# Kernel tuning notes

Hardware: AMD Instinct MI355X
Metric: run time of the kernel (lower is better)

Reference implementation:

```python
import jax, jax.numpy as jnp
import numpy as np
import math

B, T, E, H = 64, 256, 1024, 16
HD = E // H  # 64
EPS = 1e-5


def layernorm(x, g, b):
    mu = jnp.mean(x, axis=-1, keepdims=True)
    var = jnp.mean(jnp.square(x - mu), axis=-1, keepdims=True)
    return (x - mu) * jax.lax.rsqrt(var + EPS) * g + b


def setup_inputs() -> dict:
    key = jax.random.key(0)
    ks = jax.random.split(key, 10)
    s = 0.02
    return {
        "x": jax.random.normal(ks[0], (B, T, E), dtype=jnp.float32),
        "ln1_g": jnp.ones((E,), jnp.float32),
        "ln1_b": jnp.zeros((E,), jnp.float32),
        "wk": jax.random.normal(ks[1], (H, E, HD), jnp.float32) * s,
        "wq": jax.random.normal(ks[2], (H, E, HD), jnp.float32) * s,
        "wv": jax.random.normal(ks[3], (H, E, HD), jnp.float32) * s,
        "w_proj": jax.random.normal(ks[4], (E, E), jnp.float32) * s,
        "b_proj": jnp.zeros((E,), jnp.float32),
        "ln2_g": jnp.ones((E,), jnp.float32),
        "ln2_b": jnp.zeros((E,), jnp.float32),
        "w1": jax.random.normal(ks[5], (E, E), jnp.float32) * s,
        "b1": jnp.zeros((E,), jnp.float32),
        "w2": jax.random.normal(ks[6], (E, E), jnp.float32) * s,
        "b2": jnp.zeros((E,), jnp.float32),
    }


def reference(x, ln1_g, ln1_b, wk, wq, wv, w_proj, b_proj, ln2_g, ln2_b, w1, b1, w2, b2):
    # --- multi-head causal attention on LN1(x) ---
    h = layernorm(x, ln1_g, ln1_b)
    k = jnp.einsum('bte,hed->bhtd', h, wk)
    q = jnp.einsum('bte,hed->bhtd', h, wq)
    v = jnp.einsum('bte,hed->bhtd', h, wv)
    # NOTE: original computes k @ q^T (K.Q^T), not the standard Q.K^T -- kept faithful
    scores = jnp.einsum('bhtd,bhsd->bhts', k, q) / math.sqrt(HD)
    mask = jnp.tril(jnp.ones((T, T), dtype=bool))
    scores = jnp.where(mask, scores, -jnp.inf)
    attn_w = jax.nn.softmax(scores, axis=-1)  # dropout = identity in eval
    attn = jnp.einsum('bhts,bhsd->bhtd', attn_w, v)
    attn = attn.transpose(0, 2, 1, 3).reshape(B, T, E)  # concat heads
    x = x + attn @ w_proj + b_proj
    # --- feed-forward on LN2(x) ---
    h2 = layernorm(x, ln2_g, ln2_b)
    ff = jax.nn.relu(h2 @ w1 + b1) @ w2 + b2
    return x + ff
```

## Files before the change

### kernel.cpp

```cpp
#include <hip/hip_runtime.h>

typedef unsigned int u32;
typedef unsigned short u16;
typedef __attribute__((ext_vector_type(8))) short bf16x8;
typedef __attribute__((ext_vector_type(4))) float f32x4;

#define GLOBAL_AS __attribute__((address_space(1)))
#define LDS_AS    __attribute__((address_space(3)))

#define B_   64
#define T_   256
#define E_   1024
#define H_   16
#define HD_  64
#define NTOK (B_*T_)
#define K_   1024
#define LNEPS 1e-5f

__device__ __forceinline__ float bflo(u32 u){ return __uint_as_float(u << 16); }
__device__ __forceinline__ float bfhi(u32 u){ return __uint_as_float(u & 0xffff0000u); }
__device__ __forceinline__ u16 f2bf(float f){
  u32 x = __float_as_uint(f);
  u32 r = x + 0x7fffu + ((x >> 16) & 1u);
  return (u16)(r >> 16);
}
__device__ __forceinline__ u16 f2bf_trunc(float f){
  return (u16)(__float_as_uint(f) >> 16);
}
__device__ __forceinline__ u32 pack2(float a, float b){
  return (u32)f2bf(a) | ((u32)f2bf(b) << 16);
}

__device__ __forceinline__ void gload16(const u16* g, u16* l){
  __builtin_amdgcn_global_load_lds((const GLOBAL_AS void*)g, (LDS_AS void*)l, 16, 0, 0);
}

__global__ __launch_bounds__(256) void ln_bf16_kernel(
    const float* __restrict__ x, const float* __restrict__ g,
    const float* __restrict__ b, u16* __restrict__ o)
{
  int lane  = threadIdx.x & 63;
  int token = (blockIdx.x << 2) + (threadIdx.x >> 6);
  const float4* xr = (const float4*)(x + (size_t)token * E_);
  float4 v[4];
  float s = 0.f, ss = 0.f;
  #pragma unroll
  for (int i = 0; i < 4; ++i){
    v[i] = xr[lane + 64 * i];
    s += v[i].x + v[i].y + v[i].z + v[i].w;
    ss = fmaf(v[i].x, v[i].x, fmaf(v[i].y, v[i].y,
         fmaf(v[i].z, v[i].z, fmaf(v[i].w, v[i].w, ss))));
  }
  #pragma unroll
  for (int off = 32; off > 0; off >>= 1){
    s  += __shfl_xor(s,  off);
    ss += __shfl_xor(ss, off);
  }
  float mu   = s * (1.f / E_);
  float var  = ss * (1.f / E_) - mu * mu;
  float rstd = rsqrtf(var + LNEPS);
  const float4* gr = (const float4*)g;
  const float4* br = (const float4*)b;
  uint2* orow = (uint2*)(o + (size_t)token * E_);
  #pragma unroll
  for (int i = 0; i < 4; ++i){
    float4 gg = gr[lane + 64 * i], bb = br[lane + 64 * i];
    float y0 = (v[i].x - mu) * rstd * gg.x + bb.x;
    float y1 = (v[i].y - mu) * rstd * gg.y + bb.y;
    float y2 = (v[i].z - mu) * rstd * gg.z + bb.z;
    float y3 = (v[i].w - mu) * rstd * gg.w + bb.w;
    orow[lane + 64 * i] = make_uint2(pack2(y0, y1), pack2(y2, y3));
  }
}

__global__ __launch_bounds__(256) void convq_kernel(
    const float* __restrict__ wk, const float* __restrict__ wq,
    const float* __restrict__ wv, u16* __restrict__ o)
{
  __shared__ float tile[64 * 68];
  const int zh = blockIdx.x, z = zh >> 4, h = zh & 15;
  const int e0 = blockIdx.y << 6;
  const float* w = (z == 0 ? wk : z == 1 ? wq : wv) + (size_t)h * (E_ * HD_);
  const int t = threadIdx.x;
  {
    int er = t >> 2, d0 = (t & 3) << 4;
    const float4* src = (const float4*)(w + (size_t)(e0 + er) * HD_ + d0);
    #pragma unroll
    for (int i = 0; i < 4; ++i)
      *(float4*)(tile + er * 68 + d0 + 4 * i) = src[i];
  }
  __syncthreads();
  {
    int dr = t >> 2, ee = (t & 3) << 4;
    u32 wd[8];
    #pragma unroll
    for (int j = 0; j < 8; ++j)
      wd[j] = pack2(tile[(ee + 2*j) * 68 + dr], tile[(ee + 2*j + 1) * 68 + dr]);
    u16* dst = o + (size_t)(z * 1024 + h * 64 + dr) * K_ + e0 + ee;
    *(uint4*)(dst    ) = make_uint4(wd[0], wd[1], wd[2], wd[3]);
    *(uint4*)(dst + 8) = make_uint4(wd[4], wd[5], wd[6], wd[7]);
  }
}

__global__ __launch_bounds__(256) void convt_kernel(
    const float* __restrict__ w, u16* __restrict__ o)
{
  __shared__ float tile[64 * 68];
  const int n0 = blockIdx.x << 6, k0 = blockIdx.y << 6;
  const int t = threadIdx.x;
  {
    int kr = t >> 2, nn = (t & 3) << 4;
    const float4* src = (const float4*)(w + (size_t)(k0 + kr) * E_ + n0 + nn);
    #pragma unroll
    for (int i = 0; i < 4; ++i)
      *(float4*)(tile + kr * 68 + nn + 4 * i) = src[i];
  }
  __syncthreads();
  {
    int nr = t >> 2, kk = (t & 3) << 4;
    u32 wd[8];
    #pragma unroll
    for (int j = 0; j < 8; ++j)
      wd[j] = pack2(tile[(kk + 2*j) * 68 + nr], tile[(kk + 2*j + 1) * 68 + nr]);
    u16* dst = o + (size_t)(n0 + nr) * K_ + k0 + kk;
    *(uint4*)(dst    ) = make_uint4(wd[0], wd[1], wd[2], wd[3]);
    *(uint4*)(dst + 8) = make_uint4(wd[4], wd[5], wd[6], wd[7]);
  }
}

template<int MODE>
__global__ __launch_bounds__(256) void mgemm_kernel(
    const u16* __restrict__ A, const u16* __restrict__ Bt,
    const float* __restrict__ bias, const float* __restrict__ resid,
    float* __restrict__ Cf, u16* __restrict__ Cb, u16* __restrict__ Cb2)
{
  __shared__ __align__(16) u16 lds[16384];
  u16* As = lds;
  u16* Bs = lds + 8192;
  const int row0 = blockIdx.x * 128, col0 = blockIdx.y * 128;
  const int tid = threadIdx.x, lane = tid & 63;
  const int wv_ = tid >> 6, wm = wv_ >> 1, wn = wv_ & 1;
  const int l15 = lane & 15, quad = lane >> 4;

  const int srow   = tid >> 3;
  const int schunk = ((tid & 7) ^ ((tid >> 3) & 7)) << 3;
  const u16* Ag = A  + (size_t)(row0 + srow) * K_ + schunk;
  const u16* Bg = Bt + (size_t)(col0 + srow) * K_ + schunk;
  u16* Ald = As + tid * 8;
  u16* Bld = Bs + tid * 8;

  f32x4 acc[4][4];
  #pragma unroll
  for (int i = 0; i < 4; ++i)
    #pragma unroll
    for (int j = 0; j < 4; ++j)
      acc[i][j] = (f32x4){0.f, 0.f, 0.f, 0.f};

  const int mrow = wm * 64, nrow = wn * 64;
  for (int k0 = 0; k0 < K_; k0 += 64) {
    __syncthreads();
    #pragma unroll
    for (int p = 0; p < 4; ++p) {
      gload16(Ag + (size_t)(p * 32) * K_ + k0, Ald + p * 2048);
      gload16(Bg + (size_t)(p * 32) * K_ + k0, Bld + p * 2048);
    }
    __syncthreads();
    #pragma unroll
    for (int ss = 0; ss < 2; ++ss) {
      bf16x8 a[4], b[4];
      #pragma unroll
      for (int i = 0; i < 4; ++i){
        int ma = mrow + i * 16 + l15, nb = nrow + i * 16 + l15;
        a[i] = *(const bf16x8*)(As + ma * 64 + ((((ss << 2) | quad)) ^ (ma & 7)) * 8);
        b[i] = *(const bf16x8*)(Bs + nb * 64 + ((((ss << 2) | quad)) ^ (nb & 7)) * 8);
      }
      #pragma unroll
      for (int i = 0; i < 4; ++i)
        #pragma unroll
        for (int j = 0; j < 4; ++j)
          acc[i][j] = __builtin_amdgcn_mfma_f32_16x16x32_bf16(a[i], b[j], acc[i][j], 0, 0, 0);
    }
  }

  if (MODE == 1 || MODE == 3) {
    #pragma unroll
    for (int j = 0; j < 4; ++j) {
      const int n = col0 + wn * 64 + j * 16 + l15;
      float bn = bias[n];
      #pragma unroll
      for (int i = 0; i < 4; ++i)
        #pragma unroll
        for (int r = 0; r < 4; ++r) {
          const int row = row0 + wm * 64 + i * 16 + quad * 4 + r;
          size_t idx = (size_t)row * E_ + n;
          float v = acc[i][j][r] + bn;
          if (MODE == 1) Cf[idx] = v + resid[idx];
          else           Cf[idx] = v + Cf[idx];
        }
    }
    return;
  }

  __syncthreads();
  u16* ep = lds + wv_ * 4096;
  const int nb0 = col0 + wn * 64;

  if (MODE == 2) {
    #pragma unroll
    for (int j = 0; j < 4; ++j) {
      float bn = bias[nb0 + j * 16 + l15];
      #pragma unroll
      for (int i = 0; i < 4; ++i)
        #pragma unroll
        for (int r = 0; r < 4; ++r)
          ep[(i*16 + quad*4 + r) * 64 + j*16 + l15] =
              f2bf(fmaxf(acc[i][j][r] + bn, 0.f));
    }
    __syncthreads();
    const int rbase = row0 + wm * 64;
    #pragma unroll
    for (int it = 0; it < 8; ++it) {
      int tl = it * 8 + (lane >> 3), c = lane & 7;
      uint4 v = *(const uint4*)(ep + tl * 64 + c * 8);
      *(uint4*)(Cb + (size_t)(rbase + tl) * E_ + nb0 + c * 8) = v;
    }
    return;
  }

  const int z = nb0 >> 10, h = (nb0 >> 6) & 15;
  const int bb = (row0 + wm * 64) >> 8, tb0 = (row0 + wm * 64) & 255;
  if (z < 2) {
    #pragma unroll
    for (int i = 0; i < 4; ++i)
      #pragma unroll
      for (int j = 0; j < 4; ++j)
        #pragma unroll
        for (int r = 0; r < 4; ++r)
          ep[(i*16 + quad*4 + r) * 64 + j*16 + l15] = f2bf(acc[i][j][r]);
  } else {
    #pragma unroll
    for (int i = 0; i < 4; ++i)
      #pragma unroll
      for (int j = 0; j < 4; ++j)
        #pragma unroll
        for (int r = 0; r < 4; ++r) {
          int tl = i*16 + quad*4 + r, d = j*16 + l15;
          int cs = (tl >> 3) ^ (d & 7);
          ep[d * 64 + cs * 8 + (tl & 7)] = f2bf(acc[i][j][r]);
        }
  }
  __syncthreads();
  if (z < 2) {
    u16* out = (z == 0 ? Cb : Cb2) + ((size_t)(bb * H_ + h) * T_ + tb0) * HD_;
    #pragma unroll
    for (int it = 0; it < 8; ++it) {
      int tl = it * 8 + (lane >> 3), c = lane & 7;
      uint4 v = *(const uint4*)(ep + tl * 64 + c * 8);
      *(uint4*)(out + (size_t)tl * HD_ + c * 8) = v;
    }
  } else {
    u16* out = (u16*)Cf + ((size_t)(bb * H_ + h) * HD_) * T_;
    #pragma unroll
    for (int it = 0; it < 8; ++it) {
      int dl = it * 8 + (lane >> 3), c = lane & 7;
      int cs = c ^ (dl & 7);
      uint4 v = *(const uint4*)(ep + dl * 64 + cs * 8);
      *(uint4*)(out + (size_t)dl * T_ + tb0 + c * 8) = v;
    }
  }
}

__global__ __launch_bounds__(256) void fattn_kernel(
    const u16* __restrict__ kk_, const u16* __restrict__ qq_,
    const u16* __restrict__ vt_, u16* __restrict__ out)
{
  __shared__ __align__(16) u16 Pb[4][64 * 72];
  const int tid = threadIdx.x, lane = tid & 63, wv = tid >> 6;
  const int bh = blockIdx.x * 4 + wv;
  const int tblk = blockIdx.y;
  const int l15 = lane & 15, quad = lane >> 4;
  const u16* kb  = kk_ + (size_t)bh * (T_ * HD_);
  const u16* qb  = qq_ + (size_t)bh * (T_ * HD_);
  const u16* vtb = vt_ + (size_t)bh * (HD_ * T_);
  u16* Pw = Pb[wv];

  bf16x8 kf[4][2];
  #pragma unroll
  for (int i = 0; i < 4; ++i)
    #pragma unroll
    for (int c = 0; c < 2; ++c)
      kf[i][c] = *(const bf16x8*)(kb + (size_t)(tblk*64 + i*16 + l15) * HD_ + c*32 + quad*8);

  f32x4 o[4][4];
  float mrow[4][4], lrow[4][4];
  #pragma unroll
  for (int i = 0; i < 4; ++i) {
    #pragma unroll
    for (int j = 0; j < 4; ++j) o[i][j] = (f32x4){0.f, 0.f, 0.f, 0.f};
    #pragma unroll
    for (int r = 0; r < 4; ++r) { mrow[i][r] = -1e30f; lrow[i][r] = 0.f; }
  }

  for (int sb = 0; sb <= tblk; ++sb) {
    f32x4 S[4][4];
    #pragma unroll
    for (int j = 0; j < 4; ++j) {
      bf16x8 qf0 = *(const bf16x8*)(qb + (size_t)(sb*64 + j*16 + l15) * HD_ +      quad*8);
      bf16x8 qf1 = *(const bf16x8*)(qb + (size_t)(sb*64 + j*16 + l15) * HD_ + 32 + quad*8);
      #pragma unroll
      for (int i = 0; i < 4; ++i) {
        f32x4 t0 = __builtin_amdgcn_mfma_f32_16x16x32_bf16(kf[i][0], qf0,
                       (f32x4){0.f,0.f,0.f,0.f}, 0, 0, 0);
        S[i][j] = __builtin_amdgcn_mfma_f32_16x16x32_bf16(kf[i][1], qf1, t0, 0, 0, 0);
      }
    }
    #pragma unroll
    for (int i = 0; i < 4; ++i)
      #pragma unroll
      for (int j = 0; j < 4; ++j)
        #pragma unroll
        for (int r = 0; r < 4; ++r) {
          float val = S[i][j][r] * 0.125f;
          if (sb == tblk) {
            int tl = i*16 + quad*4 + r, sl = j*16 + l15;
            if (sl > tl) val = -1e30f;
          }
          S[i][j][r] = val;
        }
    #pragma unroll
    for (int i = 0; i < 4; ++i)
      #pragma unroll
      for (int r = 0; r < 4; ++r) {
        float mx = fmaxf(fmaxf(S[i][0][r], S[i][1][r]), fmaxf(S[i][2][r], S[i][3][r]));
        #pragma unroll
        for (int msk = 1; msk < 16; msk <<= 1) mx = fmaxf(mx, __shfl_xor(mx, msk));
        float mn = fmaxf(mrow[i][r], mx);
        float al = __expf(mrow[i][r] - mn);
        mrow[i][r] = mn;
        float sm = 0.f;
        #pragma unroll
        for (int j = 0; j < 4; ++j) {
          float p = __expf(S[i][j][r] - mn);
          S[i][j][r] = p;
          sm += p;
        }
        #pragma unroll
        for (int msk = 1; msk < 16; msk <<= 1) sm += __shfl_xor(sm, msk);
        lrow[i][r] = lrow[i][r] * al + sm;
        #pragma unroll
        for (int jd = 0; jd < 4; ++jd) o[i][jd][r] *= al;
      }
    #pragma unroll
    for (int i = 0; i < 4; ++i)
      #pragma unroll
      for (int j = 0; j < 4; ++j)
        #pragma unroll
        for (int r = 0; r < 4; ++r)
          Pw[(i*16 + quad*4 + r) * 72 + j*16 + l15] = f2bf_trunc(S[i][j][r]);
    __syncthreads();
    bf16x8 pf[4][2];
    #pragma unroll
    for (int i = 0; i < 4; ++i)
      #pragma unroll
      for (int c = 0; c < 2; ++c)
        pf[i][c] = *(const bf16x8*)(Pw + (i*16 + l15) * 72 + c*32 + quad*8);
    #pragma unroll
    for (int jd = 0; jd < 4; ++jd) {
      bf16x8 vf0 = *(const bf16x8*)(vtb + (size_t)(jd*16 + l15) * T_ + sb*64 +      quad*8);
      bf16x8 vf1 = *(const bf16x8*)(vtb + (size_t)(jd*16 + l15) * T_ + sb*64 + 32 + quad*8);
      #pragma unroll
      for (int i = 0; i < 4; ++i) {
        f32x4 t0 = __builtin_amdgcn_mfma_f32_16x16x32_bf16(pf[i][0], vf0, o[i][jd], 0, 0, 0);
        o[i][jd] = __builtin_amdgcn_mfma_f32_16x16x32_bf16(pf[i][1], vf1, t0, 0, 0, 0);
      }
    }
    __syncthreads();
  }

  #pragma unroll
  for (int i = 0; i < 4; ++i)
    #pragma unroll
    for (int r = 0; r < 4; ++r) {
      float inv = 1.0f / lrow[i][r];
      #pragma unroll
      for (int jd = 0; jd < 4; ++jd)
        Pw[(i*16 + quad*4 + r) * 72 + jd*16 + l15] = f2bf(o[i][jd][r] * inv);
    }
  __syncthreads();
  {
    const int b = bh >> 4, h = bh & 15;
    const uint4* pr = (const uint4*)(Pw + lane * 72);
    uint4* og = (uint4*)(out + ((size_t)(b * T_ + tblk*64 + lane)) * E_ + h * HD_);
    #pragma unroll
    for (int k = 0; k < 8; ++k) og[k] = pr[k];
  }
}

extern "C" void kernel_launch(void* const* d_in, const int* in_sizes, int n_in,
                              void* d_out, int out_size, void* d_ws, size_t ws_size,
                              hipStream_t stream) {
  const float* x     = (const float*)d_in[0];
  const float* ln1g  = (const float*)d_in[1];
  const float* ln1b  = (const float*)d_in[2];
  const float* wk    = (const float*)d_in[3];
  const float* wq    = (const float*)d_in[4];
  const float* wv    = (const float*)d_in[5];
  const float* wproj = (const float*)d_in[6];
  const float* bproj = (const float*)d_in[7];
  const float* ln2g  = (const float*)d_in[8];
  const float* ln2b  = (const float*)d_in[9];
  const float* w1    = (const float*)d_in[10];
  const float* b1    = (const float*)d_in[11];
  const float* w2    = (const float*)d_in[12];
  const float* b2    = (const float*)d_in[13];
  float* outp = (float*)d_out;

  char* ws = (char*)d_ws;
  const size_t MB = 1024 * 1024;
  u16* wqkvT  = (u16*)(ws);
  u16* wprojT = (u16*)(ws + 6 * MB);
  u16* w1T    = (u16*)(ws + 8 * MB);
  u16* w2T    = (u16*)(ws + 10 * MB);
  u16* hb     = (u16*)(ws + 16 * MB);
  u16* kbuf   = (u16*)(ws + 48 * MB);
  u16* qbuf   = (u16*)(ws + 80 * MB);
  u16* vtbuf  = (u16*)d_out;

  convq_kernel<<<dim3(48, 16), 256, 0, stream>>>(wk, wq, wv, wqkvT);
  convt_kernel<<<dim3(16, 16), 256, 0, stream>>>(wproj, wprojT);
  convt_kernel<<<dim3(16, 16), 256, 0, stream>>>(w1, w1T);
  convt_kernel<<<dim3(16, 16), 256, 0, stream>>>(w2, w2T);

  ln_bf16_kernel<<<NTOK/4, 256, 0, stream>>>(x, ln1g, ln1b, hb);
  mgemm_kernel<0><<<dim3(NTOK/128, 3*E_/128), 256, 0, stream>>>(
      hb, wqkvT, nullptr, nullptr, (float*)vtbuf, kbuf, qbuf);
  fattn_kernel<<<dim3(B_*H_/4, 4), 256, 0, stream>>>(kbuf, qbuf, vtbuf, hb);
  mgemm_kernel<1><<<dim3(NTOK/128, E_/128), 256, 0, stream>>>(
      hb, wprojT, bproj, x, outp, nullptr, nullptr);
  ln_bf16_kernel<<<NTOK/4, 256, 0, stream>>>(outp, ln2g, ln2b, kbuf);
  mgemm_kernel<2><<<dim3(NTOK/128, E_/128), 256, 0, stream>>>(
      kbuf, w1T, b1, nullptr, nullptr, qbuf, nullptr);
  mgemm_kernel<3><<<dim3(NTOK/128, E_/128), 256, 0, stream>>>(
      qbuf, w2T, b2, nullptr, outp, nullptr, nullptr);
}
```

Measured before the change: 531.7 us.

## Rewrite GEMM as 256x256 tiles with 4-stage LDS pipeline and XCD remap

Replaces the synchronous 128x128 tile GEMM with a 256x256 tile per 512-thread block. It streams K in 32-wide slices through a 4-deep LDS ring buffer, issuing async global-to-LDS loads three slices ahead and interleaving them with MFMA bursts under s_setprio and barriers. It also remaps block ids so consecutive tiles land on the same XCD for L2 reuse, and widens the epilogues to the larger tile. The goal is to hide global load latency and improve operand reuse. The cost is far more LDS (128KB) and register pressure, and fewer blocks (256 for the E-wide GEMMs), which may underfill the GPU.

```diff
diff --git a/kernel.cpp b/kernel.cpp
--- a/kernel.cpp
+++ b/kernel.cpp
@@ -128,71 +128,124 @@
   }
 }
 
+#define MF4(I, AV)                                                                 \
+  acc[I][0] = __builtin_amdgcn_mfma_f32_16x16x32_bf16(AV, b0, acc[I][0], 0, 0, 0); \
+  acc[I][1] = __builtin_amdgcn_mfma_f32_16x16x32_bf16(AV, b1, acc[I][1], 0, 0, 0); \
+  acc[I][2] = __builtin_amdgcn_mfma_f32_16x16x32_bf16(AV, b2, acc[I][2], 0, 0, 0); \
+  acc[I][3] = __builtin_amdgcn_mfma_f32_16x16x32_bf16(AV, b3, acc[I][3], 0, 0, 0);
+
+#define MG_SLICE(SLOT, DSTSLOT, KOFF, DO_STAGE, VM)                           \
+  {                                                                           \
+    const u16* As_ = lds + (SLOT) * 16384;                                    \
+    const u16* Bs_ = As_ + 8192;                                              \
+    u16* dst_ = lds + (DSTSLOT) * 16384;                                      \
+    bf16x8 b0 = *(const bf16x8*)(Bs_ + boff);                                 \
+    bf16x8 b1 = *(const bf16x8*)(Bs_ + boff + 512);                           \
+    bf16x8 b2 = *(const bf16x8*)(Bs_ + boff + 1024);                          \
+    bf16x8 b3 = *(const bf16x8*)(Bs_ + boff + 1536);                          \
+    bf16x8 a0 = *(const bf16x8*)(As_ + aoff);                                 \
+    bf16x8 a1 = *(const bf16x8*)(As_ + aoff + 512);                           \
+    bf16x8 a2 = *(const bf16x8*)(As_ + aoff + 1024);                          \
+    bf16x8 a3 = *(const bf16x8*)(As_ + aoff + 1536);                          \
+    if (DO_STAGE) {                                                           \
+      gload16(Ag0 + (KOFF), dst_ + tid * 8);                                  \
+      gload16(Ag1 + (KOFF), dst_ + 4096 + tid * 8);                           \
+    }                                                                         \
+    __builtin_amdgcn_s_barrier();                                             \
+    asm volatile("s_waitcnt lgkmcnt(0)" ::: "memory");                        \
+    __builtin_amdgcn_sched_barrier(0);                                        \
+    __builtin_amdgcn_s_setprio(1);                                            \
+    MF4(0, a0) MF4(1, a1) MF4(2, a2) MF4(3, a3)                               \
+    __builtin_amdgcn_s_setprio(0);                                            \
+    __builtin_amdgcn_s_barrier();                                             \
+    asm volatile("" ::: "memory");                                            \
+    a0 = *(const bf16x8*)(As_ + aoff + 2048);                                 \
+    a1 = *(const bf16x8*)(As_ + aoff + 2560);                                 \
+    a2 = *(const bf16x8*)(As_ + aoff + 3072);                                 \
+    a3 = *(const bf16x8*)(As_ + aoff + 3584);                                 \
+    if (DO_STAGE) {                                                           \
+      gload16(Bg0 + (KOFF), dst_ + 8192 + tid * 8);                           \
+      gload16(Bg1 + (KOFF), dst_ + 12288 + tid * 8);                          \
+    }                                                                         \
+    __builtin_amdgcn_s_barrier();                                             \
+    asm volatile("s_waitcnt lgkmcnt(0)" ::: "memory");                        \
+    __builtin_amdgcn_sched_barrier(0);                                        \
+    __builtin_amdgcn_s_setprio(1);                                            \
+    MF4(4, a0) MF4(5, a1) MF4(6, a2) MF4(7, a3)                               \
+    __builtin_amdgcn_s_setprio(0);                                            \
+    VM;                                                                       \
+    __builtin_amdgcn_s_barrier();                                             \
+    asm volatile("" ::: "memory");                                            \
+  }
+
 template<int MODE>
-__global__ __launch_bounds__(256) void mgemm_kernel(
+__global__ __launch_bounds__(512, 2) void mgemm_kernel(
     const u16* __restrict__ A, const u16* __restrict__ Bt,
     const float* __restrict__ bias, const float* __restrict__ resid,
     float* __restrict__ Cf, u16* __restrict__ Cb, u16* __restrict__ Cb2)
 {
-  __shared__ __align__(16) u16 lds[16384];
-  u16* As = lds;
-  u16* Bs = lds + 8192;
-  const int row0 = blockIdx.x * 128, col0 = blockIdx.y * 128;
-  const int tid = threadIdx.x, lane = tid & 63;
-  const int wv_ = tid >> 6, wm = wv_ >> 1, wn = wv_ & 1;
+  __shared__ __align__(16) u16 lds[65536];
+
+  const int tid = threadIdx.x, lane = tid & 63, wid = tid >> 6;
+  const int wm = wid >> 2, wn = wid & 3;
   const int l15 = lane & 15, quad = lane >> 4;
 
-  const int srow   = tid >> 3;
-  const int schunk = ((tid & 7) ^ ((tid >> 3) & 7)) << 3;
-  const u16* Ag = A  + (size_t)(row0 + srow) * K_ + schunk;
-  const u16* Bg = Bt + (size_t)(col0 + srow) * K_ + schunk;
-  u16* Ald = As + tid * 8;
-  u16* Bld = Bs + tid * 8;
-
-  f32x4 acc[4][4];
-  #pragma unroll
-  for (int i = 0; i < 4; ++i)
+  const int nwg = (int)(gridDim.x * gridDim.y);
+  int wg = (int)(blockIdx.y * gridDim.x + blockIdx.x);
+  wg = (wg & 7) * (nwg >> 3) + (wg >> 3);
+  const int row0 = (wg & 63) << 8;
+  const int col0 = (wg >> 6) << 8;
+
+  const int srow = tid >> 2;
+  const int slog = (tid & 3) ^ ((srow + (srow >> 2)) & 3);
+  const u16* Ag0 = A  + (size_t)(row0 + srow) * K_ + slog * 8;
+  const u16* Ag1 = Ag0 + (size_t)128 * K_;
+  const u16* Bg0 = Bt + (size_t)(col0 + srow) * K_ + slog * 8;
+  const u16* Bg1 = Bg0 + (size_t)128 * K_;
+
+  const int cofs = ((quad ^ ((l15 + (l15 >> 2)) & 3)) << 3);
+  const int aoff = (wm * 128 + l15) * 32 + cofs;
+  const int boff = (wn * 64  + l15) * 32 + cofs;
+
+  f32x4 acc[8][4];
+  #pragma unroll
+  for (int i = 0; i < 8; ++i)
     #pragma unroll
     for (int j = 0; j < 4; ++j)
       acc[i][j] = (f32x4){0.f, 0.f, 0.f, 0.f};
 
-  const int mrow = wm * 64, nrow = wn * 64;
-  for (int k0 = 0; k0 < K_; k0 += 64) {
-    __syncthreads();
-    #pragma unroll
-    for (int p = 0; p < 4; ++p) {
-      gload16(Ag + (size_t)(p * 32) * K_ + k0, Ald + p * 2048);
-      gload16(Bg + (size_t)(p * 32) * K_ + k0, Bld + p * 2048);
-    }
-    __syncthreads();
-    #pragma unroll
-    for (int ss = 0; ss < 2; ++ss) {
-      bf16x8 a[4], b[4];
-      #pragma unroll
-      for (int i = 0; i < 4; ++i){
-        int ma = mrow + i * 16 + l15, nb = nrow + i * 16 + l15;
-        a[i] = *(const bf16x8*)(As + ma * 64 + ((((ss << 2) | quad)) ^ (ma & 7)) * 8);
-        b[i] = *(const bf16x8*)(Bs + nb * 64 + ((((ss << 2) | quad)) ^ (nb & 7)) * 8);
-      }
-      #pragma unroll
-      for (int i = 0; i < 4; ++i)
-        #pragma unroll
-        for (int j = 0; j < 4; ++j)
-          acc[i][j] = __builtin_amdgcn_mfma_f32_16x16x32_bf16(a[i], b[j], acc[i][j], 0, 0, 0);
-    }
-  }
+  #pragma unroll
+  for (int t = 0; t < 3; ++t) {
+    u16* dst = lds + t * 16384;
+    gload16(Ag0 + t * 32, dst + tid * 8);
+    gload16(Ag1 + t * 32, dst + 4096 + tid * 8);
+    gload16(Bg0 + t * 32, dst + 8192 + tid * 8);
+    gload16(Bg1 + t * 32, dst + 12288 + tid * 8);
+  }
+  asm volatile("s_waitcnt vmcnt(8)" ::: "memory");
+  __builtin_amdgcn_s_barrier();
+  asm volatile("" ::: "memory");
+
+  #pragma unroll 1
+  for (int s = 0; s < 29; ++s)
+    MG_SLICE(s & 3, (s + 3) & 3, (s + 3) * 32, 1,
+             asm volatile("s_waitcnt vmcnt(8)" ::: "memory"))
+  MG_SLICE(1, 0, 0, 0, asm volatile("s_waitcnt vmcnt(4)" ::: "memory"))
+  MG_SLICE(2, 0, 0, 0, asm volatile("s_waitcnt vmcnt(0)" ::: "memory"))
+  MG_SLICE(3, 0, 0, 0, ((void)0))
 
   if (MODE == 1 || MODE == 3) {
+    const int rbase = row0 + wm * 128;
     #pragma unroll
     for (int j = 0; j < 4; ++j) {
       const int n = col0 + wn * 64 + j * 16 + l15;
-      float bn = bias[n];
-      #pragma unroll
-      for (int i = 0; i < 4; ++i)
+      const float bn = bias[n];
+      #pragma unroll
+      for (int i = 0; i < 8; ++i)
         #pragma unroll
         for (int r = 0; r < 4; ++r) {
-          const int row = row0 + wm * 64 + i * 16 + quad * 4 + r;
-          size_t idx = (size_t)row * E_ + n;
+          const int row = rbase + i * 16 + quad * 4 + r;
+          const size_t idx = (size_t)row * E_ + n;
           float v = acc[i][j][r] + bn;
           if (MODE == 1) Cf[idx] = v + resid[idx];
           else           Cf[idx] = v + Cf[idx];
@@ -201,71 +254,69 @@
     return;
   }
 
-  __syncthreads();
-  u16* ep = lds + wv_ * 4096;
+  u16* ep = lds + wid * 8192;
   const int nb0 = col0 + wn * 64;
 
   if (MODE == 2) {
     #pragma unroll
     for (int j = 0; j < 4; ++j) {
-      float bn = bias[nb0 + j * 16 + l15];
-      #pragma unroll
-      for (int i = 0; i < 4; ++i)
+      const float bn = bias[nb0 + j * 16 + l15];
+      #pragma unroll
+      for (int i = 0; i < 8; ++i)
         #pragma unroll
         for (int r = 0; r < 4; ++r)
           ep[(i*16 + quad*4 + r) * 64 + j*16 + l15] =
               f2bf(fmaxf(acc[i][j][r] + bn, 0.f));
     }
     __syncthreads();
-    const int rbase = row0 + wm * 64;
-    #pragma unroll
-    for (int it = 0; it < 8; ++it) {
-      int tl = it * 8 + (lane >> 3), c = lane & 7;
+    const int rbase = row0 + wm * 128;
+    #pragma unroll
+    for (int it = 0; it < 16; ++it) {
+      const int tl = it * 8 + (lane >> 3), c = lane & 7;
       uint4 v = *(const uint4*)(ep + tl * 64 + c * 8);
       *(uint4*)(Cb + (size_t)(rbase + tl) * E_ + nb0 + c * 8) = v;
     }
     return;
   }
 
-  const int z = nb0 >> 10, h = (nb0 >> 6) & 15;
-  const int bb = (row0 + wm * 64) >> 8, tb0 = (row0 + wm * 64) & 255;
+  const int z = nb0 >> 10, hh = (nb0 >> 6) & 15;
+  const int rows0 = row0 + wm * 128;
+  const int bb = rows0 >> 8, tb0 = rows0 & 255;
   if (z < 2) {
     #pragma unroll
-    for (int i = 0; i < 4; ++i)
+    for (int i = 0; i < 8; ++i)
       #pragma unroll
       for (int j = 0; j < 4; ++j)
         #pragma unroll
         for (int r = 0; r < 4; ++r)
           ep[(i*16 + quad*4 + r) * 64 + j*16 + l15] = f2bf(acc[i][j][r]);
-  } else {
-    #pragma unroll
-    for (int i = 0; i < 4; ++i)
-      #pragma unroll
-      for (int j = 0; j < 4; ++j)
-        #pragma unroll
-        for (int r = 0; r < 4; ++r) {
-          int tl = i*16 + quad*4 + r, d = j*16 + l15;
-          int cs = (tl >> 3) ^ (d & 7);
-          ep[d * 64 + cs * 8 + (tl & 7)] = f2bf(acc[i][j][r]);
-        }
-  }
-  __syncthreads();
-  if (z < 2) {
-    u16* out = (z == 0 ? Cb : Cb2) + ((size_t)(bb * H_ + h) * T_ + tb0) * HD_;
-    #pragma unroll
-    for (int it = 0; it < 8; ++it) {
-      int tl = it * 8 + (lane >> 3), c = lane & 7;
+    __syncthreads();
+    u16* out = (z == 0 ? Cb : Cb2) + ((size_t)(bb * H_ + hh) * T_ + tb0) * HD_;
+    #pragma unroll
+    for (int it = 0; it < 16; ++it) {
+      const int tl = it * 8 + (lane >> 3), c = lane & 7;
       uint4 v = *(const uint4*)(ep + tl * 64 + c * 8);
       *(uint4*)(out + (size_t)tl * HD_ + c * 8) = v;
     }
   } else {
-    u16* out = (u16*)Cf + ((size_t)(bb * H_ + h) * HD_) * T_;
-    #pragma unroll
-    for (int it = 0; it < 8; ++it) {
-      int dl = it * 8 + (lane >> 3), c = lane & 7;
-      int cs = c ^ (dl & 7);
-      uint4 v = *(const uint4*)(ep + dl * 64 + cs * 8);
-      *(uint4*)(out + (size_t)dl * T_ + tb0 + c * 8) = v;
+    #pragma unroll
+    for (int i = 0; i < 8; ++i)
+      #pragma unroll
+      for (int j = 0; j < 4; ++j)
+        #pragma unroll
+        for (int r = 0; r < 4; ++r) {
+          const int tl = i*16 + quad*4 + r, d = j*16 + l15;
+          const int phys = (tl >> 3) ^ (d & 15);
+          ep[d * 128 + phys * 8 + (tl & 7)] = f2bf(acc[i][j][r]);
+        }
+    __syncthreads();
+    u16* out = (u16*)Cf + ((size_t)(bb * H_ + hh) * HD_) * T_;
+    #pragma unroll
+    for (int it = 0; it < 16; ++it) {
+      const int d = it * 4 + (lane >> 4), c = lane & 15;
+      const int phys = c ^ (d & 15);
+      uint4 v = *(const uint4*)(ep + d * 128 + phys * 8);
+      *(uint4*)(out + (size_t)d * T_ + tb0 + c * 8) = v;
     }
   }
 }
@@ -432,14 +483,14 @@
   convt_kernel<<<dim3(16, 16), 256, 0, stream>>>(w2, w2T);
 
   ln_bf16_kernel<<<NTOK/4, 256, 0, stream>>>(x, ln1g, ln1b, hb);
-  mgemm_kernel<0><<<dim3(NTOK/128, 3*E_/128), 256, 0, stream>>>(
+  mgemm_kernel<0><<<dim3(64, 12), 512, 0, stream>>>(
       hb, wqkvT, nullptr, nullptr, (float*)vtbuf, kbuf, qbuf);
   fattn_kernel<<<dim3(B_*H_/4, 4), 256, 0, stream>>>(kbuf, qbuf, vtbuf, hb);
-  mgemm_kernel<1><<<dim3(NTOK/128, E_/128), 256, 0, stream>>>(
+  mgemm_kernel<1><<<dim3(64, 4), 512, 0, stream>>>(
       hb, wprojT, bproj, x, outp, nullptr, nullptr);
   ln_bf16_kernel<<<NTOK/4, 256, 0, stream>>>(outp, ln2g, ln2b, kbuf);
-  mgemm_kernel<2><<<dim3(NTOK/128, E_/128), 256, 0, stream>>>(
+  mgemm_kernel<2><<<dim3(64, 4), 512, 0, stream>>>(
       kbuf, w1T, b1, nullptr, nullptr, qbuf, nullptr);
-  mgemm_kernel<3><<<dim3(NTOK/128, E_/128), 256, 0, stream>>>(
+  mgemm_kernel<3><<<dim3(64, 4), 512, 0, stream>>>(
       qbuf, w2T, b2, nullptr, outp, nullptr, nullptr);
 }
```

New measurement: 545.0 us. 1.03x slower.
